# Performance work log

Hardware: AMD Instinct MI355X
Metric: run time of the kernel (lower is better)

## Reference

```python
import jax, jax.numpy as jnp
import numpy as np

D_MODEL = 1024
NUM_HEADS = 16
HEAD_DIM = D_MODEL // NUM_HEADS


def setup_inputs() -> dict:
    key = jax.random.key(0)
    ks = jax.random.split(key, 9)
    s = 1.0 / np.sqrt(D_MODEL)  # torch Linear default init range scale
    def lin(k):
        kw, kb = jax.random.split(k)
        W = jax.random.uniform(kw, (D_MODEL, D_MODEL), jnp.float32, -s, s)
        b = jax.random.uniform(kb, (D_MODEL,), jnp.float32, -s, s)
        return W, b
    Wq, bq = lin(ks[0])
    Wk, bk = lin(ks[1])
    Wv, bv = lin(ks[2])
    Wo, bo = lin(ks[3])
    x = jax.random.normal(ks[4], (4, 2048, D_MODEL), jnp.float32)
    return {"x": x, "Wq": Wq, "bq": bq, "Wk": Wk, "bk": bk,
            "Wv": Wv, "bv": bv, "Wo": Wo, "bo": bo}


def reference(x, Wq, bq, Wk, bk, Wv, bv, Wo, bo):
    B, S, _ = x.shape
    H, Dh = NUM_HEADS, HEAD_DIM
    scale = Dh ** -0.5
    # projections; W stored as [in, out] so y = x @ W + b
    q = (x @ Wq + bq).reshape(B, S, H, Dh).transpose(0, 2, 1, 3)  # [B,H,S,Dh]
    k = (x @ Wk + bk).reshape(B, S, H, Dh).transpose(0, 2, 1, 3)
    v = (x @ Wv + bv).reshape(B, S, H, Dh).transpose(0, 2, 1, 3)
    scores = jnp.einsum('bhqd,bhkd->bhqk', q, k) * scale  # [B,H,S,S]
    causal = jnp.tril(jnp.ones((S, S), dtype=bool))
    scores = jnp.where(causal[None, None], scores, jnp.finfo(scores.dtype).min)
    attn = jax.nn.softmax(scores, axis=-1)
    out = jnp.einsum('bhqk,bhkd->bhqd', attn, v)  # [B,H,S,Dh]
    out = out.transpose(0, 2, 1, 3).reshape(B, S, H * Dh)
    return out @ Wo + bo
```

## Files before the change

kernel.cpp:

```cpp
#include <hip/hip_runtime.h>
#include <math.h>

#define DM 1024
#define NH 16
#define DH 64
#define BB 4
#define SS 2048
#define MROWS (BB*SS)

typedef __bf16 bf16;
typedef __bf16 bf16x2 __attribute__((ext_vector_type(2)));
typedef __bf16 bf16x8 __attribute__((ext_vector_type(8)));
typedef float floatx4 __attribute__((ext_vector_type(4)));
typedef float floatx16 __attribute__((ext_vector_type(16)));
typedef unsigned int uintx4 __attribute__((ext_vector_type(4)));
typedef unsigned int uintx2 __attribute__((ext_vector_type(2)));

#if __has_builtin(__builtin_amdgcn_exp2f)
#define EXP2F __builtin_amdgcn_exp2f
#else
#define EXP2F exp2f
#endif

#define QSCALE (0.125f * 1.44269504088896f)

__device__ __forceinline__ void cp16(void* lds, const void* g) {
  __builtin_amdgcn_global_load_lds(
      (__attribute__((address_space(1))) void*)(void*)g,
      (__attribute__((address_space(3))) void*)lds,
      16, 0, 0);
}

__device__ __forceinline__ unsigned pk2(float a, float b) {
  bf16x2 t;
  t[0] = (bf16)a;
  t[1] = (bf16)b;
  return __builtin_bit_cast(unsigned, t);
}

#if __has_builtin(__builtin_amdgcn_permlane32_swap)
__device__ __forceinline__ void pl32(unsigned& a, unsigned& b) {
  uintx2 r = __builtin_amdgcn_permlane32_swap(a, b, false, false);
  a = r[0]; b = r[1];
}
#else
__device__ __forceinline__ void pl32(unsigned& a, unsigned& b) {
  asm volatile("v_permlane32_swap_b32 %0, %1" : "+v"(a), "+v"(b));
}
#endif

__global__ __launch_bounds__(256) void cvt_x(
    const float* __restrict__ X, bf16* __restrict__ Y) {
  int i = (blockIdx.x * 256 + threadIdx.x) * 8;
  float4 a = *(const float4*)&X[i];
  float4 b = *(const float4*)&X[i + 4];
  bf16x8 o;
  o[0] = (bf16)a.x; o[1] = (bf16)a.y; o[2] = (bf16)a.z; o[3] = (bf16)a.w;
  o[4] = (bf16)b.x; o[5] = (bf16)b.y; o[6] = (bf16)b.z; o[7] = (bf16)b.w;
  *(bf16x8*)&Y[i] = o;
}

__global__ __launch_bounds__(1024) void wtransc(
    const float* __restrict__ W0, const float* __restrict__ W1,
    const float* __restrict__ W2, const float* __restrict__ W3,
    bf16* __restrict__ T0, bf16* __restrict__ T1,
    bf16* __restrict__ T2, bf16* __restrict__ T3) {
  __shared__ float tile[32][33];
  const float* W; bf16* T;
  int z = blockIdx.z;
  if (z == 0)      { W = W0; T = T0; }
  else if (z == 1) { W = W1; T = T1; }
  else if (z == 2) { W = W2; T = T2; }
  else             { W = W3; T = T3; }
  int tx = threadIdx.x, ty = threadIdx.y;
  tile[ty][tx] = W[(blockIdx.y * 32 + ty) * DM + blockIdx.x * 32 + tx];
  __syncthreads();
  T[(blockIdx.x * 32 + ty) * DM + blockIdx.y * 32 + tx] = (bf16)tile[tx][ty];
}

#define BK 32

__global__ __launch_bounds__(512, 1) void gemm_qkv(
    const bf16* __restrict__ A, const bf16* __restrict__ WT,
    const float* __restrict__ bq, const float* __restrict__ bk,
    const float* __restrict__ bv,
    bf16* __restrict__ qb, bf16* __restrict__ kb, bf16* __restrict__ vt) {
  __shared__ __align__(16) char smem[(2 * 256 * 64 + 2 * 128 * 64) * 2];
  bf16* Ab = (bf16*)smem;
  bf16* Bb = (bf16*)(smem + 2 * 256 * 64 * 2);
  bf16* Ts = (bf16*)smem;

  int tid = threadIdx.x;
  int lane = tid & 63, w = tid >> 6;
  int wr = w >> 1, wc = w & 1;
  int qd = lane >> 4, l15 = lane & 15;

  int bid = blockIdx.x;
  int xcd = bid & 7, rr_ = bid >> 3;
  int mb = rr_ & 31, nb = xcd * 3 + (rr_ >> 5);
  int m0 = mb * 256;
  int n0 = nb * 128;
  int which = n0 >> 10;

  floatx4 acc[4][4] = {};

  auto stageA = [&](int pb, int t, int hf) {
    for (int i = 0; i < 2; ++i) {
      int L = i * 512 + tid;
      int row = L >> 3, ch = L & 7;
      int sch = ch ^ (row & 7);
      cp16(&Ab[pb * 256 * 64 + (hf * 128 + row) * 64 + ch * 8],
           &A[(size_t)(m0 + hf * 128 + row) * DM + t * 64 + sch * 8]);
    }
  };
  auto stageB = [&](int pb, int t) {
    for (int i = 0; i < 2; ++i) {
      int L = i * 512 + tid;
      int row = L >> 3, ch = L & 7;
      int sch = ch ^ (row & 7);
      cp16(&Bb[pb * 128 * 64 + row * 64 + ch * 8],
           &WT[(size_t)(n0 + row) * DM + t * 64 + sch * 8]);
    }
  };
  auto ldA = [&](int pb, int mt, int ks) -> bf16x8 {
    int row = wr * 64 + mt * 16 + l15;
    int c = ((ks << 2) + qd) ^ (row & 7);
    return *(const bf16x8*)&Ab[pb * 256 * 64 + row * 64 + c * 8];
  };
  auto ldB = [&](int pb, int nt, int ks) -> bf16x8 {
    int row = wc * 64 + nt * 16 + l15;
    int c = ((ks << 2) + qd) ^ (row & 7);
    return *(const bf16x8*)&Bb[pb * 128 * 64 + row * 64 + c * 8];
  };

  stageA(0, 0, 0);
  stageA(0, 0, 1);
  stageB(0, 0);
  stageB(1, 1);
  asm volatile("s_waitcnt vmcnt(2)" ::: "memory");
  __builtin_amdgcn_s_barrier();

  for (int g = 0; g < 16; ++g) {
    int pb = g & 1;
    bf16x8 af0[2][2], bfr[4][2];
    for (int mt = 0; mt < 2; ++mt)
      for (int ks = 0; ks < 2; ++ks) af0[mt][ks] = ldA(pb, mt, ks);
    for (int nt = 0; nt < 4; ++nt)
      for (int ks = 0; ks < 2; ++ks) bfr[nt][ks] = ldB(pb, nt, ks);
    if (g + 1 < 16) { stageA(pb ^ 1, g + 1, 0); stageA(pb ^ 1, g + 1, 1); }
    __builtin_amdgcn_s_barrier();
    asm volatile("s_waitcnt lgkmcnt(0)" ::: "memory");
    __builtin_amdgcn_sched_barrier(0);
    __builtin_amdgcn_s_setprio(1);
    for (int mt = 0; mt < 2; ++mt)
      for (int nt = 0; nt < 4; ++nt)
        for (int ks = 0; ks < 2; ++ks)
          acc[mt][nt] = __builtin_amdgcn_mfma_f32_16x16x32_bf16(
              af0[mt][ks], bfr[nt][ks], acc[mt][nt], 0, 0, 0);
    __builtin_amdgcn_s_setprio(0);
    __builtin_amdgcn_s_barrier();
    bf16x8 af1[2][2];
    for (int mt = 0; mt < 2; ++mt)
      for (int ks = 0; ks < 2; ++ks) af1[mt][ks] = ldA(pb, 2 + mt, ks);
    if (g + 2 < 16) stageB(pb, g + 2);
    __builtin_amdgcn_s_barrier();
    asm volatile("s_waitcnt lgkmcnt(0)" ::: "memory");
    __builtin_amdgcn_sched_barrier(0);
    __builtin_amdgcn_s_setprio(1);
    for (int mt = 0; mt < 2; ++mt)
      for (int nt = 0; nt < 4; ++nt)
        for (int ks = 0; ks < 2; ++ks)
          acc[2 + mt][nt] = __builtin_amdgcn_mfma_f32_16x16x32_bf16(
              af1[mt][ks], bfr[nt][ks], acc[2 + mt][nt], 0, 0, 0);
    __builtin_amdgcn_s_setprio(0);
    if (g < 14)
      asm volatile("s_waitcnt vmcnt(2)" ::: "memory");
    else if (g == 14)
      asm volatile("s_waitcnt vmcnt(0)" ::: "memory");
    __builtin_amdgcn_s_barrier();
  }

  __syncthreads();

  const float* bias = (which == 0) ? bq : (which == 1) ? bk : bv;

  if (which == 2) {
    for (int nt = 0; nt < 4; ++nt) {
      int dl = wc * 64 + nt * 16 + l15;
      float bv_ = bias[(n0 & 1023) + dl];
      for (int mt = 0; mt < 4; ++mt)
        for (int r = 0; r < 4; ++r)
          Ts[dl * 264 + wr * 64 + mt * 16 + qd * 4 + r] =
              (bf16)(acc[mt][nt][r] + bv_);
    }
    __syncthreads();
    int dl = tid >> 2, s0 = (tid & 3) * 64;
    size_t vrow = (size_t)((n0 & 1023) + dl) * MROWS + m0 + s0;
    for (int j = 0; j < 8; ++j)
      *(bf16x8*)&vt[vrow + j * 8] = *(const bf16x8*)&Ts[dl * 264 + s0 + j * 8];
  } else {
    bf16* out = (which == 0) ? qb : kb;
    float sc = (which == 0) ? QSCALE : 1.0f;
    for (int nt = 0; nt < 4; ++nt) {
      int col = (n0 & 1023) + wc * 64 + nt * 16 + l15;
      float bv_ = bias[col];
      for (int mt = 0; mt < 4; ++mt)
        for (int r = 0; r < 4; ++r) {
          int row = m0 + wr * 64 + mt * 16 + qd * 4 + r;
          out[(size_t)row * DM + col] = (bf16)((acc[mt][nt][r] + bv_) * sc);
        }
    }
  }
}

__global__ __launch_bounds__(512, 1) void gemm_out(
    const bf16* __restrict__ A, const bf16* __restrict__ WT,
    const float* __restrict__ bias, float* __restrict__ C) {
  __shared__ __align__(16) char smem[(2 * 256 * 64 + 2 * 128 * 64) * 2];
  bf16* Ab = (bf16*)smem;
  bf16* Bb = (bf16*)(smem + 2 * 256 * 64 * 2);

  int tid = threadIdx.x;
  int lane = tid & 63, w = tid >> 6;
  int wr = w >> 1, wc = w & 1;
  int qd = lane >> 4, l15 = lane & 15;

  int bid = blockIdx.x;
  int m0 = (bid >> 3) * 256;
  int n0 = (bid & 7) * 128;

  floatx4 acc[4][4] = {};

  auto stageA = [&](int pb, int t, int hf) {
    for (int i = 0; i < 2; ++i) {
      int L = i * 512 + tid;
      int row = L >> 3, ch = L & 7;
      int sch = ch ^ (row & 7);
      cp16(&Ab[pb * 256 * 64 + (hf * 128 + row) * 64 + ch * 8],
           &A[(size_t)(m0 + hf * 128 + row) * DM + t * 64 + sch * 8]);
    }
  };
  auto stageB = [&](int pb, int t) {
    for (int i = 0; i < 2; ++i) {
      int L = i * 512 + tid;
      int row = L >> 3, ch = L & 7;
      int sch = ch ^ (row & 7);
      cp16(&Bb[pb * 128 * 64 + row * 64 + ch * 8],
           &WT[(size_t)(n0 + row) * DM + t * 64 + sch * 8]);
    }
  };
  auto ldA = [&](int pb, int mt, int ks) -> bf16x8 {
    int row = wr * 64 + mt * 16 + l15;
    int c = ((ks << 2) + qd) ^ (row & 7);
    return *(const bf16x8*)&Ab[pb * 256 * 64 + row * 64 + c * 8];
  };
  auto ldB = [&](int pb, int nt, int ks) -> bf16x8 {
    int row = wc * 64 + nt * 16 + l15;
    int c = ((ks << 2) + qd) ^ (row & 7);
    return *(const bf16x8*)&Bb[pb * 128 * 64 + row * 64 + c * 8];
  };

  stageA(0, 0, 0);
  stageA(0, 0, 1);
  stageB(0, 0);
  stageB(1, 1);
  asm volatile("s_waitcnt vmcnt(2)" ::: "memory");
  __builtin_amdgcn_s_barrier();

  for (int g = 0; g < 16; ++g) {
    int pb = g & 1;
    bf16x8 af0[2][2], bfr[4][2];
    for (int mt = 0; mt < 2; ++mt)
      for (int ks = 0; ks < 2; ++ks) af0[mt][ks] = ldA(pb, mt, ks);
    for (int nt = 0; nt < 4; ++nt)
      for (int ks = 0; ks < 2; ++ks) bfr[nt][ks] = ldB(pb, nt, ks);
    if (g + 1 < 16) { stageA(pb ^ 1, g + 1, 0); stageA(pb ^ 1, g + 1, 1); }
    __builtin_amdgcn_s_barrier();
    asm volatile("s_waitcnt lgkmcnt(0)" ::: "memory");
    __builtin_amdgcn_sched_barrier(0);
    __builtin_amdgcn_s_setprio(1);
    for (int mt = 0; mt < 2; ++mt)
      for (int nt = 0; nt < 4; ++nt)
        for (int ks = 0; ks < 2; ++ks)
          acc[mt][nt] = __builtin_amdgcn_mfma_f32_16x16x32_bf16(
              af0[mt][ks], bfr[nt][ks], acc[mt][nt], 0, 0, 0);
    __builtin_amdgcn_s_setprio(0);
    __builtin_amdgcn_s_barrier();
    bf16x8 af1[2][2];
    for (int mt = 0; mt < 2; ++mt)
      for (int ks = 0; ks < 2; ++ks) af1[mt][ks] = ldA(pb, 2 + mt, ks);
    if (g + 2 < 16) stageB(pb, g + 2);
    __builtin_amdgcn_s_barrier();
    asm volatile("s_waitcnt lgkmcnt(0)" ::: "memory");
    __builtin_amdgcn_sched_barrier(0);
    __builtin_amdgcn_s_setprio(1);
    for (int mt = 0; mt < 2; ++mt)
      for (int nt = 0; nt < 4; ++nt)
        for (int ks = 0; ks < 2; ++ks)
          acc[2 + mt][nt] = __builtin_amdgcn_mfma_f32_16x16x32_bf16(
              af1[mt][ks], bfr[nt][ks], acc[2 + mt][nt], 0, 0, 0);
    __builtin_amdgcn_s_setprio(0);
    if (g < 14)
      asm volatile("s_waitcnt vmcnt(2)" ::: "memory");
    else if (g == 14)
      asm volatile("s_waitcnt vmcnt(0)" ::: "memory");
    __builtin_amdgcn_s_barrier();
  }

  for (int nt = 0; nt < 4; ++nt) {
    int col = n0 + wc * 64 + nt * 16 + l15;
    float bv_ = bias[col];
    for (int mt = 0; mt < 4; ++mt)
      for (int r = 0; r < 4; ++r) {
        int row = m0 + wr * 64 + mt * 16 + qd * 4 + r;
        C[(size_t)row * DM + col] = acc[mt][nt][r] + bv_;
      }
  }
}

__global__ __launch_bounds__(256, 2) void attn_fwd(
    const bf16* __restrict__ Qg, const bf16* __restrict__ Kg,
    const bf16* __restrict__ Vt, bf16* __restrict__ O) {
  __shared__ __align__(16) bf16 Kbuf[3][64 * 64];
  __shared__ __align__(16) bf16 Vbuf[3][64 * 64];

  int tid = threadIdx.x;
  int lane = tid & 63, w = tid >> 6;
  int q31 = lane & 31, hi = lane >> 5;
  int pair = blockIdx.x, h = blockIdx.y, b = blockIdx.z;
  int base = b * SS;
  int hoff = h * DH;

  auto stage = [&](int bi, int kt) {
    int kbase = base + kt * 64;
    for (int i = 0; i < 2; ++i) {
      int c = i * 256 + tid;
      int row = c >> 3;
      int sch = (c & 7) ^ (row & 7);
      cp16(&Kbuf[bi][c * 8], &Kg[(size_t)(kbase + row) * DM + hoff + sch * 8]);
      cp16(&Vbuf[bi][c * 8],
           &Vt[(size_t)(hoff + row) * MROWS + base + kt * 64 + sch * 8]);
    }
  };

  int swz = q31 & 7;

  for (int ph = 0; ph < 2; ++ph) {
    int jt = ph ? (15 - pair) : pair;
    int q0 = jt * 128;
    int nkt = 2 * jt + 2;

    stage(0, 0);
    stage(1, 1);

    int rowq = q0 + w * 32 + q31;
    bf16x8 qf[4];
    for (int ds = 0; ds < 4; ++ds)
      qf[ds] = *(const bf16x8*)
          &Qg[(size_t)(base + rowq) * DM + hoff + ds * 16 + hi * 8];

    float lacc = 0.0f;
    floatx16 oacc0 = {}, oacc1 = {};

    asm volatile("s_waitcnt vmcnt(8)" ::: "memory");
    __builtin_amdgcn_s_barrier();

    int bi = 0;
    for (int kt = 0; kt < nkt; ++kt) {
      if (kt + 2 < nkt) stage((bi + 2) % 3, kt + 2);

      floatx16 sA = {}, sB = {};
      __builtin_amdgcn_s_setprio(1);
      for (int ds = 0; ds < 4; ++ds) {
        bf16x8 kfA = *(const bf16x8*)
            &Kbuf[bi][(q31)*64 + (((ds << 1) + hi) ^ swz) * 8];
        bf16x8 kfB = *(const bf16x8*)
            &Kbuf[bi][(32 + q31) * 64 + (((ds << 1) + hi) ^ swz) * 8];
        sA = __builtin_amdgcn_mfma_f32_32x32x16_bf16(kfA, qf[ds], sA, 0, 0, 0);
        sB = __builtin_amdgcn_mfma_f32_32x32x16_bf16(kfB, qf[ds], sB, 0, 0, 0);
      }
      __builtin_amdgcn_s_setprio(0);

      if (kt >= 2 * jt) {
#pragma unroll
        for (int r = 0; r < 16; ++r) {
          int key = kt * 64 + (r & 3) + 8 * (r >> 2) + 4 * hi;
          if (key > rowq) sA[r] = -3e38f;
          if (key + 32 > rowq) sB[r] = -3e38f;
        }
      }

      float pA[16], pB[16];
#pragma unroll
      for (int r = 0; r < 16; ++r) {
        pA[r] = EXP2F(sA[r]);
        pB[r] = EXP2F(sB[r]);
      }
      float s0 = 0.f, s1 = 0.f, s2 = 0.f, s3 = 0.f;
#pragma unroll
      for (int r = 0; r < 16; r += 2) {
        s0 += pA[r]; s1 += pA[r + 1];
        s2 += pB[r]; s3 += pB[r + 1];
      }
      lacc += (s0 + s1) + (s2 + s3);

      bf16x8 pf[4];
      {
        unsigned w0 = pk2(pA[0], pA[1]), w2 = pk2(pA[4], pA[5]);
        unsigned w1 = pk2(pA[2], pA[3]), w3 = pk2(pA[6], pA[7]);
        pl32(w0, w2); pl32(w1, w3);
        uintx4 ww; ww[0] = w0; ww[1] = w1; ww[2] = w2; ww[3] = w3;
        pf[0] = __builtin_bit_cast(bf16x8, ww);
        w0 = pk2(pA[8], pA[9]);  w2 = pk2(pA[12], pA[13]);
        w1 = pk2(pA[10], pA[11]); w3 = pk2(pA[14], pA[15]);
        pl32(w0, w2); pl32(w1, w3);
        ww[0] = w0; ww[1] = w1; ww[2] = w2; ww[3] = w3;
        pf[1] = __builtin_bit_cast(bf16x8, ww);
        w0 = pk2(pB[0], pB[1]);  w2 = pk2(pB[4], pB[5]);
        w1 = pk2(pB[2], pB[3]);  w3 = pk2(pB[6], pB[7]);
        pl32(w0, w2); pl32(w1, w3);
        ww[0] = w0; ww[1] = w1; ww[2] = w2; ww[3] = w3;
        pf[2] = __builtin_bit_cast(bf16x8, ww);
        w0 = pk2(pB[8], pB[9]);  w2 = pk2(pB[12], pB[13]);
        w1 = pk2(pB[10], pB[11]); w3 = pk2(pB[14], pB[15]);
        pl32(w0, w2); pl32(w1, w3);
        ww[0] = w0; ww[1] = w1; ww[2] = w2; ww[3] = w3;
        pf[3] = __builtin_bit_cast(bf16x8, ww);
      }

      __builtin_amdgcn_s_setprio(1);
#pragma unroll
      for (int s4 = 0; s4 < 4; ++s4) {
        bf16x8 vf0 = *(const bf16x8*)
            &Vbuf[bi][(q31)*64 + (((s4 << 1) + hi) ^ swz) * 8];
        bf16x8 vf1 = *(const bf16x8*)
            &Vbuf[bi][(32 + q31) * 64 + (((s4 << 1) + hi) ^ swz) * 8];
        oacc0 = __builtin_amdgcn_mfma_f32_32x32x16_bf16(pf[s4], vf0, oacc0, 0, 0, 0);
        oacc1 = __builtin_amdgcn_mfma_f32_32x32x16_bf16(pf[s4], vf1, oacc1, 0, 0, 0);
      }
      __builtin_amdgcn_s_setprio(0);

      int rem = nkt - 1 - kt;
      if (rem >= 2) {
        asm volatile("s_waitcnt vmcnt(8)" ::: "memory");
        __builtin_amdgcn_s_barrier();
      } else if (rem == 1) {
        asm volatile("s_waitcnt vmcnt(0)" ::: "memory");
        __builtin_amdgcn_s_barrier();
      }
      bi = (bi == 2) ? 0 : bi + 1;
    }

    __syncthreads();

    lacc += __shfl_xor(lacc, 32, 64);
#pragma unroll
    for (int r = 0; r < 16; ++r) {
      int rr = (r & 3) + 8 * (r >> 2) + 4 * hi;
      float inv = 1.0f / __shfl(lacc, rr, 64);
      size_t row = (size_t)(base + q0 + w * 32 + rr) * DM + hoff;
      O[row + q31] = (bf16)(oacc0[r] * inv);
      O[row + 32 + q31] = (bf16)(oacc1[r] * inv);
    }
  }
}

extern "C" void kernel_launch(void* const* d_in, const int* in_sizes, int n_in,
                              void* d_out, int out_size, void* d_ws, size_t ws_size,
                              hipStream_t stream) {
  const float* x  = (const float*)d_in[0];
  const float* Wq = (const float*)d_in[1];
  const float* bq = (const float*)d_in[2];
  const float* Wk = (const float*)d_in[3];
  const float* bk = (const float*)d_in[4];
  const float* Wv = (const float*)d_in[5];
  const float* bv = (const float*)d_in[6];
  const float* Wo = (const float*)d_in[7];
  const float* bo = (const float*)d_in[8];
  float* out = (float*)d_out;

  char* ws = (char*)d_ws;
  const size_t act = (size_t)MROWS * DM * sizeof(bf16);
  bf16* xb    = (bf16*)(ws);
  bf16* qb    = (bf16*)(ws + act);
  bf16* kb    = (bf16*)(ws + 2 * act);
  bf16* vt    = (bf16*)(ws + 3 * act);
  bf16* ab    = (bf16*)(ws + 4 * act);
  bf16* WqkvT = (bf16*)(ws + 5 * act);
  bf16* WoT   = WqkvT + 3 * (size_t)DM * DM;

  cvt_x<<<MROWS * DM / (256 * 8), 256, 0, stream>>>(x, xb);
  wtransc<<<dim3(32, 32, 4), dim3(32, 32), 0, stream>>>(
      Wq, Wk, Wv, Wo,
      WqkvT, WqkvT + (size_t)DM * DM, WqkvT + 2 * (size_t)DM * DM, WoT);

  gemm_qkv<<<768, 512, 0, stream>>>(
      xb, WqkvT, bq, bk, bv, qb, kb, vt);

  attn_fwd<<<dim3(8, NH, BB), 256, 0, stream>>>(qb, kb, vt, ab);

  gemm_out<<<256, 512, 0, stream>>>(ab, WoT, bo, out);
}
```

Measured before the change: 274.2 us.

## Fuse input conversion and weight transpose into one prep kernel; remap QKV tiles

Merges the x-to-bf16 conversion and the four-weight transpose/convert kernels into a single launch. The transpose now uses 256-thread blocks, each handling four rows per thread. The QKV GEMM block-to-tile mapping changes so each XCD gets a contiguous range of 96 tiles covering 4 M-blocks across all 24 N-blocks, instead of 32 M-blocks over 3 N-blocks. The goal is to save one launch gap and improve L2 reuse of A tiles per XCD, at the cost of reusing less of the weight tiles.

```diff
diff --git a/kernel.cpp b/kernel.cpp
--- a/kernel.cpp
+++ b/kernel.cpp
@@ -49,36 +49,45 @@
 }
 #endif
 
-__global__ __launch_bounds__(256) void cvt_x(
-    const float* __restrict__ X, bf16* __restrict__ Y) {
-  int i = (blockIdx.x * 256 + threadIdx.x) * 8;
-  float4 a = *(const float4*)&X[i];
-  float4 b = *(const float4*)&X[i + 4];
-  bf16x8 o;
-  o[0] = (bf16)a.x; o[1] = (bf16)a.y; o[2] = (bf16)a.z; o[3] = (bf16)a.w;
-  o[4] = (bf16)b.x; o[5] = (bf16)b.y; o[6] = (bf16)b.z; o[7] = (bf16)b.w;
-  *(bf16x8*)&Y[i] = o;
-}
-
-__global__ __launch_bounds__(1024) void wtransc(
+__global__ __launch_bounds__(256) void prep(
+    const float* __restrict__ X, bf16* __restrict__ Y,
     const float* __restrict__ W0, const float* __restrict__ W1,
     const float* __restrict__ W2, const float* __restrict__ W3,
     bf16* __restrict__ T0, bf16* __restrict__ T1,
     bf16* __restrict__ T2, bf16* __restrict__ T3) {
+  int bid = blockIdx.x, tid = threadIdx.x;
+  if (bid < 4096) {
+    int i = (bid * 256 + tid) * 8;
+    float4 a = *(const float4*)&X[i];
+    float4 b = *(const float4*)&X[i + 4];
+    bf16x8 o;
+    o[0] = (bf16)a.x; o[1] = (bf16)a.y; o[2] = (bf16)a.z; o[3] = (bf16)a.w;
+    o[4] = (bf16)b.x; o[5] = (bf16)b.y; o[6] = (bf16)b.z; o[7] = (bf16)b.w;
+    *(bf16x8*)&Y[i] = o;
+    return;
+  }
   __shared__ float tile[32][33];
+  int bq = bid - 4096;
+  int z = bq >> 10, rem = bq & 1023;
+  int by = rem >> 5, bx = rem & 31;
   const float* W; bf16* T;
-  int z = blockIdx.z;
   if (z == 0)      { W = W0; T = T0; }
   else if (z == 1) { W = W1; T = T1; }
   else if (z == 2) { W = W2; T = T2; }
   else             { W = W3; T = T3; }
-  int tx = threadIdx.x, ty = threadIdx.y;
-  tile[ty][tx] = W[(blockIdx.y * 32 + ty) * DM + blockIdx.x * 32 + tx];
+  int tx = tid & 31, ty4 = tid >> 5;
+#pragma unroll
+  for (int rr = 0; rr < 4; ++rr) {
+    int ty = ty4 + rr * 8;
+    tile[ty][tx] = W[(by * 32 + ty) * DM + bx * 32 + tx];
+  }
   __syncthreads();
-  T[(blockIdx.x * 32 + ty) * DM + blockIdx.y * 32 + tx] = (bf16)tile[tx][ty];
-}
-
-#define BK 32
+#pragma unroll
+  for (int rr = 0; rr < 4; ++rr) {
+    int ty = ty4 + rr * 8;
+    T[(bx * 32 + ty) * DM + by * 32 + tx] = (bf16)tile[tx][ty];
+  }
+}
 
 __global__ __launch_bounds__(512, 1) void gemm_qkv(
     const bf16* __restrict__ A, const bf16* __restrict__ WT,
@@ -96,8 +105,8 @@
   int qd = lane >> 4, l15 = lane & 15;
 
   int bid = blockIdx.x;
-  int xcd = bid & 7, rr_ = bid >> 3;
-  int mb = rr_ & 31, nb = xcd * 3 + (rr_ >> 5);
+  int wg = (bid & 7) * 96 + (bid >> 3);
+  int mb = wg / 24, nb = wg % 24;
   int m0 = mb * 256;
   int n0 = nb * 128;
   int which = n0 >> 10;
@@ -489,9 +498,8 @@
   bf16* WqkvT = (bf16*)(ws + 5 * act);
   bf16* WoT   = WqkvT + 3 * (size_t)DM * DM;
 
-  cvt_x<<<MROWS * DM / (256 * 8), 256, 0, stream>>>(x, xb);
-  wtransc<<<dim3(32, 32, 4), dim3(32, 32), 0, stream>>>(
-      Wq, Wk, Wv, Wo,
+  prep<<<8192, 256, 0, stream>>>(
+      x, xb, Wq, Wk, Wv, Wo,
       WqkvT, WqkvT + (size_t)DM * DM, WqkvT + 2 * (size_t)DM * DM, WoT);
 
   gemm_qkv<<<768, 512, 0, stream>>>(
```

New measurement: 254.1 us. -7.3%, faster.
